# Kernel tuning notes

Hardware: AMD Instinct MI355X
Metric: run time of the kernel (lower is better)

## Reference

```python
import jax, jax.numpy as jnp
import numpy as np

# irreps_in = irreps_out = 512x0e + 256x1o + 128x2e
# gate.irreps_in (= lin output) = 896x0e (512 scalars + 384 gates) + 256x1o + 128x2e
MUL0, MUL1, MUL2 = 512, 256, 128
D_S = MUL0                      # flat scalar dim in x
D_V = MUL1 * 3                  # flat 1o dim
D_T = MUL2 * 5                  # flat 2e dim
N_GATES = MUL1 + MUL2           # one sigmoid gate per l>0 channel


def setup_inputs() -> dict:
    key = jax.random.key(0)
    k1, k2, k3, k4 = jax.random.split(key, 4)
    N = 50000
    x = jax.random.normal(k1, (N, D_S + D_V + D_T), dtype=jnp.float32)
    W0 = jax.random.normal(k2, (MUL0, MUL0 + N_GATES), dtype=jnp.float32)
    W1 = jax.random.normal(k3, (MUL1, MUL1), dtype=jnp.float32)
    W2 = jax.random.normal(k4, (MUL2, MUL2), dtype=jnp.float32)
    return {"x": x, "W0": W0, "W1": W1, "W2": W2}


def reference(x, W0, W1, W2):
    N = x.shape[0]
    # split flat features into irrep blocks
    s = x[:, :D_S]                                   # [N, 512]   0e scalars
    v = x[:, D_S:D_S + D_V].reshape(N, MUL1, 3)      # [N, 256, 3] 1o
    t = x[:, D_S + D_V:].reshape(N, MUL2, 5)         # [N, 128, 5] 2e

    # e3nn o3.Linear: per-irrep channel mixing, element normalization 1/sqrt(fan_in)
    s_out = (s @ W0) / jnp.sqrt(jnp.asarray(MUL0, x.dtype))        # [N, 896]
    v_out = jnp.einsum('nim,io->nom', v, W1) / jnp.sqrt(jnp.asarray(MUL1, x.dtype))
    t_out = jnp.einsum('nim,io->nom', t, W2) / jnp.sqrt(jnp.asarray(MUL2, x.dtype))

    # Gate: LeakyReLU on even scalars, sigmoid gates broadcast over l>0 blocks
    scalars = jax.nn.leaky_relu(s_out[:, :MUL0])                   # [N, 512]
    gates = jax.nn.sigmoid(s_out[:, MUL0:])                        # [N, 384]
    gv = v_out * gates[:, :MUL1, None]                             # [N, 256, 3]
    gt = t_out * gates[:, MUL1:, None]                             # [N, 128, 5]

    return jnp.concatenate([scalars, gv.reshape(N, -1), gt.reshape(N, -1)], axis=-1)
```

## Files before the change

kernel.cpp:

```cpp
#include <hip/hip_runtime.h>


typedef unsigned short u16;
typedef short bf16x8 __attribute__((ext_vector_type(8)));
typedef float f32x4 __attribute__((ext_vector_type(4)));

#define ROWLEN 1920

__device__ __forceinline__ u16 f2bf(float f) {
  unsigned int u = __float_as_uint(f);
  u += 0x7fffu + ((u >> 16) & 1u);
  return (u16)(u >> 16);
}

__device__ __forceinline__ float sigmoid_f(float x) {
  return 1.0f / (1.0f + __expf(-x));
}

__global__ __launch_bounds__(256) void prep_kernel(
    const float* __restrict__ W0, const float* __restrict__ W1,
    const float* __restrict__ W2, u16* __restrict__ WT0,
    u16* __restrict__ WT1, u16* __restrict__ WT2) {
  int idx = blockIdx.x * 256 + threadIdx.x;
  if (idx < 896 * 512) {
    int n = idx >> 9, k = idx & 511;
    WT0[idx] = f2bf(W0[k * 896 + n]);
    return;
  }
  int j = idx - 896 * 512;
  if (j >= 0 && j < 256 * 256) {
    int o = j >> 8, i = j & 255;
    WT1[j] = f2bf(W1[i * 256 + o]);
    return;
  }
  int j2 = idx - (896 * 512 + 256 * 256);
  if (j2 >= 0 && j2 < 128 * 128) {
    int o = j2 >> 7, i = j2 & 127;
    WT2[j2] = f2bf(W2[i * 128 + o]);
  }
}

__global__ __launch_bounds__(256) void s_kernel(
    const float* __restrict__ x, const u16* __restrict__ WT0,
    float* __restrict__ out, int N) {
  const int r0 = blockIdx.x * 128;
  const int n0 = blockIdx.y * 128;
  __shared__ __align__(16) u16 As[128 * 72];
  __shared__ __align__(16) u16 Bs[128 * 72];

  const int tid = threadIdx.x;
  const int lane = tid & 63, wid = tid >> 6;
  const int wm = wid & 1, wn = wid >> 1;
  const int lm = lane & 15, lq = lane >> 4;

  f32x4 acc[4][4];
  const f32x4 zero4 = {0.f, 0.f, 0.f, 0.f};
#pragma unroll
  for (int i = 0; i < 4; ++i)
#pragma unroll
    for (int j = 0; j < 4; ++j) acc[i][j] = zero4;

  const int ac = tid & 15;
  const int ar = tid >> 4;
  const int bg = tid & 15;
  const int bn = tid >> 4;

  for (int k0 = 0; k0 < 512; k0 += 64) {
    float4 va[8];
#pragma unroll
    for (int p = 0; p < 8; ++p) {
      int rr = ar + p * 16;
      int rg = r0 + rr; if (rg >= N) rg = N - 1;
      va[p] = *(const float4*)(x + (size_t)rg * ROWLEN + k0 + ac * 4);
    }
    ushort4 vb[8];
#pragma unroll
    for (int p = 0; p < 8; ++p) {
      int nn = bn + p * 16;
      vb[p] = *(const ushort4*)(WT0 + (size_t)(n0 + nn) * 512 + k0 + bg * 4);
    }
#pragma unroll
    for (int p = 0; p < 8; ++p) {
      int rr = ar + p * 16;
      ushort4 h;
      h.x = f2bf(va[p].x); h.y = f2bf(va[p].y);
      h.z = f2bf(va[p].z); h.w = f2bf(va[p].w);
      *(ushort4*)&As[rr * 72 + ac * 4] = h;
    }
#pragma unroll
    for (int p = 0; p < 8; ++p) {
      int nn = bn + p * 16;
      *(ushort4*)&Bs[nn * 72 + bg * 4] = vb[p];
    }
    __syncthreads();

#pragma unroll
    for (int kk = 0; kk < 64; kk += 32) {
      bf16x8 af[4], bfr[4];
#pragma unroll
      for (int mt = 0; mt < 4; ++mt)
        af[mt] = *(const bf16x8*)&As[(wm * 64 + mt * 16 + lm) * 72 + kk + lq * 8];
#pragma unroll
      for (int nt = 0; nt < 4; ++nt)
        bfr[nt] = *(const bf16x8*)&Bs[(wn * 64 + nt * 16 + lm) * 72 + kk + lq * 8];
#pragma unroll
      for (int mt = 0; mt < 4; ++mt)
#pragma unroll
        for (int nt = 0; nt < 4; ++nt)
          acc[mt][nt] = __builtin_amdgcn_mfma_f32_16x16x32_bf16(
              af[mt], bfr[nt], acc[mt][nt], 0, 0, 0);
    }
    __syncthreads();
  }

  const float scale = 0.04419417382415922f;
#pragma unroll
  for (int mt = 0; mt < 4; ++mt) {
#pragma unroll
    for (int reg = 0; reg < 4; ++reg) {
      int row = r0 + wm * 64 + mt * 16 + lq * 4 + reg;
      if (row >= N) continue;
      float* orow = out + (size_t)row * ROWLEN;
#pragma unroll
      for (int nt = 0; nt < 4; ++nt) {
        int col = n0 + wn * 64 + nt * 16 + lm;
        float v = acc[mt][nt][reg] * scale;
        float r = (col < 512) ? (v > 0.f ? v : 0.01f * v)
                              : sigmoid_f(v);
        orow[col] = r;
      }
    }
  }
}

__global__ __launch_bounds__(256) void v_kernel(
    const float* __restrict__ x, const u16* __restrict__ WT1,
    float* __restrict__ out, int N) {
  const int r0 = blockIdx.x * 32;
  __shared__ __align__(16) u16 Av[3 * 32 * 72];
  __shared__ __align__(16) u16 Bs[256 * 72];

  const int tid = threadIdx.x;
  const int lane = tid & 63, w = tid >> 6;
  const int lm = lane & 15, lq = lane >> 4;

  f32x4 acc[3][2][4];
  const f32x4 zero4 = {0.f, 0.f, 0.f, 0.f};
#pragma unroll
  for (int m = 0; m < 3; ++m)
#pragma unroll
    for (int i = 0; i < 2; ++i)
#pragma unroll
      for (int j = 0; j < 4; ++j) acc[m][i][j] = zero4;

  const int arr = tid >> 3;
  const int ag = tid & 7;
  const int bg = tid & 15, bn = tid >> 4;

  for (int k0 = 0; k0 < 256; k0 += 64) {
    {
      int rg = r0 + arr; if (rg >= N) rg = N - 1;
      const float* src = x + (size_t)rg * ROWLEN + 512 + 3 * k0;
#pragma unroll
      for (int it = 0; it < 6; ++it) {
        int c4 = ag + it * 8;
        float4 v = *(const float4*)(src + c4 * 4);
        float tmp[4] = {v.x, v.y, v.z, v.w};
#pragma unroll
        for (int jj = 0; jj < 4; ++jj) {
          int j = c4 * 4 + jj;
          int i = j / 3, m = j % 3;
          Av[m * 2304 + arr * 72 + i] = f2bf(tmp[jj]);
        }
      }
    }
#pragma unroll
    for (int p = 0; p < 16; ++p) {
      int nn = bn + p * 16;
      *(ushort4*)&Bs[nn * 72 + bg * 4] =
          *(const ushort4*)(WT1 + (size_t)nn * 256 + k0 + bg * 4);
    }
    __syncthreads();

#pragma unroll
    for (int kk = 0; kk < 64; kk += 32) {
      bf16x8 bfr[4];
#pragma unroll
      for (int nt = 0; nt < 4; ++nt)
        bfr[nt] = *(const bf16x8*)&Bs[(w * 64 + nt * 16 + lm) * 72 + kk + lq * 8];
#pragma unroll
      for (int m = 0; m < 3; ++m) {
        bf16x8 af[2];
#pragma unroll
        for (int mt = 0; mt < 2; ++mt)
          af[mt] = *(const bf16x8*)&Av[m * 2304 + (mt * 16 + lm) * 72 + kk + lq * 8];
#pragma unroll
        for (int mt = 0; mt < 2; ++mt)
#pragma unroll
          for (int nt = 0; nt < 4; ++nt)
            acc[m][mt][nt] = __builtin_amdgcn_mfma_f32_16x16x32_bf16(
                af[mt], bfr[nt], acc[m][mt][nt], 0, 0, 0);
      }
    }
    __syncthreads();
  }

  float g[2][4][4];
#pragma unroll
  for (int mt = 0; mt < 2; ++mt) {
#pragma unroll
    for (int reg = 0; reg < 4; ++reg) {
      int row = r0 + mt * 16 + lq * 4 + reg;
      int rc = row < N ? row : (N - 1);
#pragma unroll
      for (int nt = 0; nt < 4; ++nt) {
        int o = w * 64 + nt * 16 + lm;
        g[mt][reg][nt] = out[(size_t)rc * ROWLEN + 512 + o];
      }
    }
  }
  asm volatile("s_waitcnt vmcnt(0)" ::: "memory");
  __syncthreads();

  const float scale = 0.0625f;
#pragma unroll
  for (int mt = 0; mt < 2; ++mt) {
#pragma unroll
    for (int reg = 0; reg < 4; ++reg) {
      int row = r0 + mt * 16 + lq * 4 + reg;
      if (row >= N) continue;
#pragma unroll
      for (int nt = 0; nt < 4; ++nt) {
        int o = w * 64 + nt * 16 + lm;
        float* p = out + (size_t)row * ROWLEN + 512 + 3 * o;
        float gg = g[mt][reg][nt];
        p[0] = acc[0][mt][nt][reg] * scale * gg;
        p[1] = acc[1][mt][nt][reg] * scale * gg;
        p[2] = acc[2][mt][nt][reg] * scale * gg;
      }
    }
  }
}

__global__ __launch_bounds__(256) void t_kernel(
    const float* __restrict__ x, const u16* __restrict__ WT2,
    float* __restrict__ out, int N) {
  const int r0 = blockIdx.x * 32;
  __shared__ __align__(16) u16 Av[5 * 32 * 72];
  __shared__ __align__(16) u16 Bs[128 * 72];

  const int tid = threadIdx.x;
  const int lane = tid & 63, w = tid >> 6;
  const int lm = lane & 15, lq = lane >> 4;

  f32x4 acc[5][2][2];
  const f32x4 zero4 = {0.f, 0.f, 0.f, 0.f};
#pragma unroll
  for (int m = 0; m < 5; ++m)
#pragma unroll
    for (int i = 0; i < 2; ++i)
#pragma unroll
      for (int j = 0; j < 2; ++j) acc[m][i][j] = zero4;

  const int arr = tid >> 3;
  const int ag = tid & 7;
  const int bg = tid & 15, bn = tid >> 4;

  for (int k0 = 0; k0 < 128; k0 += 64) {
    {
      int rg = r0 + arr; if (rg >= N) rg = N - 1;
      const float* src = x + (size_t)rg * ROWLEN + 1280 + 5 * k0;
#pragma unroll
      for (int it = 0; it < 10; ++it) {
        int c4 = ag + it * 8;
        float4 v = *(const float4*)(src + c4 * 4);
        float tmp[4] = {v.x, v.y, v.z, v.w};
#pragma unroll
        for (int jj = 0; jj < 4; ++jj) {
          int j = c4 * 4 + jj;
          int i = j / 5, m = j % 5;
          Av[m * 2304 + arr * 72 + i] = f2bf(tmp[jj]);
        }
      }
    }
#pragma unroll
    for (int p = 0; p < 8; ++p) {
      int nn = bn + p * 16;
      *(ushort4*)&Bs[nn * 72 + bg * 4] =
          *(const ushort4*)(WT2 + (size_t)nn * 128 + k0 + bg * 4);
    }
    __syncthreads();

#pragma unroll
    for (int kk = 0; kk < 64; kk += 32) {
      bf16x8 bfr[2];
#pragma unroll
      for (int nt = 0; nt < 2; ++nt)
        bfr[nt] = *(const bf16x8*)&Bs[(w * 32 + nt * 16 + lm) * 72 + kk + lq * 8];
#pragma unroll
      for (int m = 0; m < 5; ++m) {
        bf16x8 af[2];
#pragma unroll
        for (int mt = 0; mt < 2; ++mt)
          af[mt] = *(const bf16x8*)&Av[m * 2304 + (mt * 16 + lm) * 72 + kk + lq * 8];
#pragma unroll
        for (int mt = 0; mt < 2; ++mt)
#pragma unroll
          for (int nt = 0; nt < 2; ++nt)
            acc[m][mt][nt] = __builtin_amdgcn_mfma_f32_16x16x32_bf16(
                af[mt], bfr[nt], acc[m][mt][nt], 0, 0, 0);
      }
    }
    __syncthreads();
  }

  const float scale = 0.08838834764831845f;
#pragma unroll
  for (int mt = 0; mt < 2; ++mt) {
#pragma unroll
    for (int reg = 0; reg < 4; ++reg) {
      int row = r0 + mt * 16 + lq * 4 + reg;
      if (row >= N) continue;
#pragma unroll
      for (int nt = 0; nt < 2; ++nt) {
        int o = w * 32 + nt * 16 + lm;
        float g = out[(size_t)row * ROWLEN + 768 + o];
        float* p = out + (size_t)row * ROWLEN + 1280 + 5 * o;
#pragma unroll
        for (int m = 0; m < 5; ++m)
          p[m] = acc[m][mt][nt][reg] * scale * g;
      }
    }
  }
}

extern "C" void kernel_launch(void* const* d_in, const int* in_sizes, int n_in,
                              void* d_out, int out_size, void* d_ws, size_t ws_size,
                              hipStream_t stream) {
  const float* x  = (const float*)d_in[0];
  const float* W0 = (const float*)d_in[1];
  const float* W1 = (const float*)d_in[2];
  const float* W2 = (const float*)d_in[3];
  float* out = (float*)d_out;
  const int N = in_sizes[0] / ROWLEN;

  u16* WT0 = (u16*)d_ws;
  u16* WT1 = WT0 + 896 * 512;
  u16* WT2 = WT1 + 256 * 256;

  prep_kernel<<<(896 * 512 + 256 * 256 + 128 * 128 + 255) / 256, 256, 0, stream>>>(
      W0, W1, W2, WT0, WT1, WT2);

  dim3 sgrid((N + 127) / 128, 7);
  s_kernel<<<sgrid, 256, 0, stream>>>(x, WT0, out, N);

  const int rb32 = (N + 31) / 32;
  t_kernel<<<rb32, 256, 0, stream>>>(x, WT2, out, N);
  v_kernel<<<rb32, 256, 0, stream>>>(x, WT1, out, N);
}
```

Before: 788.5 us.

## Use direct global-to-LDS loads with XOR swizzle and 512-thread blocks in v/t kernels

The v and t kernels now stage weight tiles with global_load_lds 16-byte direct-to-LDS transfers into an XOR-swizzled unpadded layout, replacing register-staged ushort4 copies. Blocks double to 512 threads (8 waves split 2x4 over rows and columns), which halves per-wave accumulators and spreads the x-tile conversion across more threads. The aim is less VGPR pressure and instruction overhead on the loads and higher occupancy. The risk is extra LDS traffic per block and more complex swizzle addressing.

```diff
diff --git a/kernel.cpp b/kernel.cpp
--- a/kernel.cpp
+++ b/kernel.cpp
@@ -15,6 +15,12 @@
 
 __device__ __forceinline__ float sigmoid_f(float x) {
   return 1.0f / (1.0f + __expf(-x));
+}
+
+__device__ __forceinline__ void gload_lds16(const void* g, void* l) {
+  __builtin_amdgcn_global_load_lds(
+      (const __attribute__((address_space(1))) unsigned int*)g,
+      (__attribute__((address_space(3))) unsigned int*)l, 16, 0, 0);
 }
 
 __global__ __launch_bounds__(256) void prep_kernel(
@@ -133,37 +139,42 @@
   }
 }
 
-__global__ __launch_bounds__(256) void v_kernel(
+__global__ __launch_bounds__(512, 6) void v_kernel(
     const float* __restrict__ x, const u16* __restrict__ WT1,
     float* __restrict__ out, int N) {
   const int r0 = blockIdx.x * 32;
   __shared__ __align__(16) u16 Av[3 * 32 * 72];
-  __shared__ __align__(16) u16 Bs[256 * 72];
+  __shared__ __align__(16) u16 Bs[256 * 64];
 
   const int tid = threadIdx.x;
   const int lane = tid & 63, w = tid >> 6;
   const int lm = lane & 15, lq = lane >> 4;
-
-  f32x4 acc[3][2][4];
+  const int wr = w & 1, wc = w >> 1;
+
+  f32x4 acc[3][4];
   const f32x4 zero4 = {0.f, 0.f, 0.f, 0.f};
 #pragma unroll
   for (int m = 0; m < 3; ++m)
 #pragma unroll
-    for (int i = 0; i < 2; ++i)
-#pragma unroll
-      for (int j = 0; j < 4; ++j) acc[m][i][j] = zero4;
-
-  const int arr = tid >> 3;
-  const int ag = tid & 7;
-  const int bg = tid & 15, bn = tid >> 4;
+    for (int j = 0; j < 4; ++j) acc[m][j] = zero4;
+
+  const int arr = tid >> 4;
+  const int ag = tid & 15;
 
   for (int k0 = 0; k0 < 256; k0 += 64) {
+#pragma unroll
+    for (int c = 0; c < 4; ++c) {
+      int gidx = tid + c * 512;
+      int n = gidx >> 3, kb = gidx & 7;
+      gload_lds16(WT1 + (size_t)n * 256 + k0 + ((kb ^ (n & 7)) << 3),
+                  &Bs[gidx * 8]);
+    }
     {
       int rg = r0 + arr; if (rg >= N) rg = N - 1;
       const float* src = x + (size_t)rg * ROWLEN + 512 + 3 * k0;
 #pragma unroll
-      for (int it = 0; it < 6; ++it) {
-        int c4 = ag + it * 8;
+      for (int it = 0; it < 3; ++it) {
+        int c4 = ag + it * 16;
         float4 v = *(const float4*)(src + c4 * 4);
         float tmp[4] = {v.x, v.y, v.z, v.w};
 #pragma unroll
@@ -174,49 +185,37 @@
         }
       }
     }
-#pragma unroll
-    for (int p = 0; p < 16; ++p) {
-      int nn = bn + p * 16;
-      *(ushort4*)&Bs[nn * 72 + bg * 4] =
-          *(const ushort4*)(WT1 + (size_t)nn * 256 + k0 + bg * 4);
-    }
     __syncthreads();
 
 #pragma unroll
     for (int kk = 0; kk < 64; kk += 32) {
       bf16x8 bfr[4];
 #pragma unroll
-      for (int nt = 0; nt < 4; ++nt)
-        bfr[nt] = *(const bf16x8*)&Bs[(w * 64 + nt * 16 + lm) * 72 + kk + lq * 8];
+      for (int nt = 0; nt < 4; ++nt) {
+        int n = wc * 64 + nt * 16 + lm;
+        bfr[nt] = *(const bf16x8*)&Bs[n * 64 + ((kk + lq * 8) ^ ((n & 7) << 3))];
+      }
 #pragma unroll
       for (int m = 0; m < 3; ++m) {
-        bf16x8 af[2];
-#pragma unroll
-        for (int mt = 0; mt < 2; ++mt)
-          af[mt] = *(const bf16x8*)&Av[m * 2304 + (mt * 16 + lm) * 72 + kk + lq * 8];
-#pragma unroll
-        for (int mt = 0; mt < 2; ++mt)
-#pragma unroll
-          for (int nt = 0; nt < 4; ++nt)
-            acc[m][mt][nt] = __builtin_amdgcn_mfma_f32_16x16x32_bf16(
-                af[mt], bfr[nt], acc[m][mt][nt], 0, 0, 0);
-      }
-    }
-    __syncthreads();
-  }
-
-  float g[2][4][4];
-#pragma unroll
-  for (int mt = 0; mt < 2; ++mt) {
-#pragma unroll
-    for (int reg = 0; reg < 4; ++reg) {
-      int row = r0 + mt * 16 + lq * 4 + reg;
-      int rc = row < N ? row : (N - 1);
-#pragma unroll
-      for (int nt = 0; nt < 4; ++nt) {
-        int o = w * 64 + nt * 16 + lm;
-        g[mt][reg][nt] = out[(size_t)rc * ROWLEN + 512 + o];
-      }
+        bf16x8 af = *(const bf16x8*)&Av[m * 2304 + (wr * 16 + lm) * 72 + kk + lq * 8];
+#pragma unroll
+        for (int nt = 0; nt < 4; ++nt)
+          acc[m][nt] = __builtin_amdgcn_mfma_f32_16x16x32_bf16(
+              af, bfr[nt], acc[m][nt], 0, 0, 0);
+      }
+    }
+    __syncthreads();
+  }
+
+  float g[4][4];
+#pragma unroll
+  for (int reg = 0; reg < 4; ++reg) {
+    int row = r0 + wr * 16 + lq * 4 + reg;
+    int rc = row < N ? row : (N - 1);
+#pragma unroll
+    for (int nt = 0; nt < 4; ++nt) {
+      int o = wc * 64 + nt * 16 + lm;
+      g[reg][nt] = out[(size_t)rc * ROWLEN + 512 + o];
     }
   }
   asm volatile("s_waitcnt vmcnt(0)" ::: "memory");
@@ -224,55 +223,57 @@
 
   const float scale = 0.0625f;
 #pragma unroll
-  for (int mt = 0; mt < 2; ++mt) {
-#pragma unroll
-    for (int reg = 0; reg < 4; ++reg) {
-      int row = r0 + mt * 16 + lq * 4 + reg;
-      if (row >= N) continue;
-#pragma unroll
-      for (int nt = 0; nt < 4; ++nt) {
-        int o = w * 64 + nt * 16 + lm;
-        float* p = out + (size_t)row * ROWLEN + 512 + 3 * o;
-        float gg = g[mt][reg][nt];
-        p[0] = acc[0][mt][nt][reg] * scale * gg;
-        p[1] = acc[1][mt][nt][reg] * scale * gg;
-        p[2] = acc[2][mt][nt][reg] * scale * gg;
-      }
-    }
-  }
-}
-
-__global__ __launch_bounds__(256) void t_kernel(
+  for (int reg = 0; reg < 4; ++reg) {
+    int row = r0 + wr * 16 + lq * 4 + reg;
+    if (row >= N) continue;
+#pragma unroll
+    for (int nt = 0; nt < 4; ++nt) {
+      int o = wc * 64 + nt * 16 + lm;
+      float* p = out + (size_t)row * ROWLEN + 512 + 3 * o;
+      float gg = g[reg][nt];
+      p[0] = acc[0][nt][reg] * scale * gg;
+      p[1] = acc[1][nt][reg] * scale * gg;
+      p[2] = acc[2][nt][reg] * scale * gg;
+    }
+  }
+}
+
+__global__ __launch_bounds__(512, 6) void t_kernel(
     const float* __restrict__ x, const u16* __restrict__ WT2,
     float* __restrict__ out, int N) {
   const int r0 = blockIdx.x * 32;
   __shared__ __align__(16) u16 Av[5 * 32 * 72];
-  __shared__ __align__(16) u16 Bs[128 * 72];
+  __shared__ __align__(16) u16 Bs[128 * 64];
 
   const int tid = threadIdx.x;
   const int lane = tid & 63, w = tid >> 6;
   const int lm = lane & 15, lq = lane >> 4;
-
-  f32x4 acc[5][2][2];
+  const int wr = w & 1, wc = w >> 1;
+
+  f32x4 acc[5][2];
   const f32x4 zero4 = {0.f, 0.f, 0.f, 0.f};
 #pragma unroll
   for (int m = 0; m < 5; ++m)
 #pragma unroll
-    for (int i = 0; i < 2; ++i)
-#pragma unroll
-      for (int j = 0; j < 2; ++j) acc[m][i][j] = zero4;
-
-  const int arr = tid >> 3;
-  const int ag = tid & 7;
-  const int bg = tid & 15, bn = tid >> 4;
+    for (int j = 0; j < 2; ++j) acc[m][j] = zero4;
+
+  const int arr = tid >> 4;
+  const int ag = tid & 15;
 
   for (int k0 = 0; k0 < 128; k0 += 64) {
+#pragma unroll
+    for (int c = 0; c < 2; ++c) {
+      int gidx = tid + c * 512;
+      int n = gidx >> 3, kb = gidx & 7;
+      gload_lds16(WT2 + (size_t)n * 128 + k0 + ((kb ^ (n & 7)) << 3),
+                  &Bs[gidx * 8]);
+    }
     {
       int rg = r0 + arr; if (rg >= N) rg = N - 1;
       const float* src = x + (size_t)rg * ROWLEN + 1280 + 5 * k0;
 #pragma unroll
-      for (int it = 0; it < 10; ++it) {
-        int c4 = ag + it * 8;
+      for (int it = 0; it < 5; ++it) {
+        int c4 = ag + it * 16;
         float4 v = *(const float4*)(src + c4 * 4);
         float tmp[4] = {v.x, v.y, v.z, v.w};
 #pragma unroll
@@ -283,32 +284,23 @@
         }
       }
     }
-#pragma unroll
-    for (int p = 0; p < 8; ++p) {
-      int nn = bn + p * 16;
-      *(ushort4*)&Bs[nn * 72 + bg * 4] =
-          *(const ushort4*)(WT2 + (size_t)nn * 128 + k0 + bg * 4);
-    }
     __syncthreads();
 
 #pragma unroll
     for (int kk = 0; kk < 64; kk += 32) {
       bf16x8 bfr[2];
 #pragma unroll
-      for (int nt = 0; nt < 2; ++nt)
-        bfr[nt] = *(const bf16x8*)&Bs[(w * 32 + nt * 16 + lm) * 72 + kk + lq * 8];
+      for (int nt = 0; nt < 2; ++nt) {
+        int n = wc * 32 + nt * 16 + lm;
+        bfr[nt] = *(const bf16x8*)&Bs[n * 64 + ((kk + lq * 8) ^ ((n & 7) << 3))];
+      }
 #pragma unroll
       for (int m = 0; m < 5; ++m) {
-        bf16x8 af[2];
-#pragma unroll
-        for (int mt = 0; mt < 2; ++mt)
-          af[mt] = *(const bf16x8*)&Av[m * 2304 + (mt * 16 + lm) * 72 + kk + lq * 8];
-#pragma unroll
-        for (int mt = 0; mt < 2; ++mt)
-#pragma unroll
-          for (int nt = 0; nt < 2; ++nt)
-            acc[m][mt][nt] = __builtin_amdgcn_mfma_f32_16x16x32_bf16(
-                af[mt], bfr[nt], acc[m][mt][nt], 0, 0, 0);
+        bf16x8 af = *(const bf16x8*)&Av[m * 2304 + (wr * 16 + lm) * 72 + kk + lq * 8];
+#pragma unroll
+        for (int nt = 0; nt < 2; ++nt)
+          acc[m][nt] = __builtin_amdgcn_mfma_f32_16x16x32_bf16(
+              af, bfr[nt], acc[m][nt], 0, 0, 0);
       }
     }
     __syncthreads();
@@ -316,20 +308,17 @@
 
   const float scale = 0.08838834764831845f;
 #pragma unroll
-  for (int mt = 0; mt < 2; ++mt) {
-#pragma unroll
-    for (int reg = 0; reg < 4; ++reg) {
-      int row = r0 + mt * 16 + lq * 4 + reg;
-      if (row >= N) continue;
-#pragma unroll
-      for (int nt = 0; nt < 2; ++nt) {
-        int o = w * 32 + nt * 16 + lm;
-        float g = out[(size_t)row * ROWLEN + 768 + o];
-        float* p = out + (size_t)row * ROWLEN + 1280 + 5 * o;
-#pragma unroll
-        for (int m = 0; m < 5; ++m)
-          p[m] = acc[m][mt][nt][reg] * scale * g;
-      }
+  for (int reg = 0; reg < 4; ++reg) {
+    int row = r0 + wr * 16 + lq * 4 + reg;
+    if (row >= N) continue;
+#pragma unroll
+    for (int nt = 0; nt < 2; ++nt) {
+      int o = wc * 32 + nt * 16 + lm;
+      float gg = out[(size_t)row * ROWLEN + 768 + o];
+      float* p = out + (size_t)row * ROWLEN + 1280 + 5 * o;
+#pragma unroll
+      for (int m = 0; m < 5; ++m)
+        p[m] = acc[m][nt][reg] * scale * gg;
     }
   }
 }
@@ -355,6 +344,6 @@
   s_kernel<<<sgrid, 256, 0, stream>>>(x, WT0, out, N);
 
   const int rb32 = (N + 31) / 32;
-  t_kernel<<<rb32, 256, 0, stream>>>(x, WT2, out, N);
-  v_kernel<<<rb32, 256, 0, stream>>>(x, WT1, out, N);
-}
+  t_kernel<<<rb32, 512, 0, stream>>>(x, WT2, out, N);
+  v_kernel<<<rb32, 512, 0, stream>>>(x, WT1, out, N);
+}
```

Result: slower. 892.1 us (+13.1%).
